# Optimization experiments

Measured on AMD Instinct MI355X. Metric: run time of the kernel, lower is better.

The kernel has to match this reference:

```python
import jax, jax.numpy as jnp
import numpy as np

N, E, B = 4096, 32768, 1024
NF, EF = 32, 16
ENC, HID, HEADS = 64, 128, 4  # hidden_dim = 2*encoder_dim
MAX_SIZE = 10


def setup_inputs() -> dict:
    key = jax.random.key(0)
    ks = jax.random.split(key, 11)
    return {
        "node_features": jax.random.normal(ks[0], (N, NF), jnp.float32),
        "edge_features": jax.random.normal(ks[1], (E, EF), jnp.float32),
        "edge_index": jax.random.randint(ks[2], (2, E), 0, N, jnp.int32),
        "current_state": jax.random.randint(ks[3], (B,), 0, N, jnp.int32),
        "n_states": jax.random.randint(ks[4], (N,), 1, MAX_SIZE + 1, jnp.int32),
        "W_h": jax.random.normal(ks[5], (NF, HID), jnp.float32) / np.sqrt(NF),
        "W_e": jax.random.normal(ks[6], (EF, HID), jnp.float32) / np.sqrt(EF),
        "W_a": jax.random.normal(ks[7], (5 * HID, HEADS * HID), jnp.float32) / np.sqrt(5 * HID),
        "W_m": jax.random.normal(ks[8], (3 * HID, HEADS * HID), jnp.float32) / np.sqrt(3 * HID),
        "a_kern": jax.random.normal(ks[9], (HID, 1), jnp.float32) / np.sqrt(HID),
        "W_g": jax.random.normal(ks[10], (HID, ENC), jnp.float32) / np.sqrt(HID),
    }


def reference(node_features, edge_features, edge_index, current_state, n_states,
              W_h, W_e, W_a, W_m, a_kern, W_g):
    n_nodes = node_features.shape[0]
    h0 = node_features @ W_h                        # [N, HID]
    e = edge_features @ W_e                         # [E, HID]
    attn_mask = jnp.any(edge_features != 0, axis=-1)  # [E]
    src, tgt = edge_index[0], edge_index[1]
    neg_inf = -jnp.inf
    h = h0
    for i in range(MAX_SIZE):
        node_in = jnp.concatenate([h, h0], axis=-1)  # [N, 2*HID]
        sf = node_in[src]                            # [E, 2*HID]
        tf = node_in[tgt]                            # [E, 2*HID]
        h_a = (jnp.concatenate([sf, e, tf], axis=-1) @ W_a).reshape(-1, HEADS, HID)
        h_m = (jnp.concatenate([e, tf], axis=-1) @ W_m).reshape(-1, HEADS, HID)
        logits = jax.nn.leaky_relu(h_a, 0.2) @ a_kern            # [E, HEADS, 1]
        logits = jnp.where(attn_mask[:, None, None], logits, neg_inf)
        max_per_node = jax.ops.segment_max(logits.reshape(logits.shape[0], -1), src,
                                           num_segments=n_nodes)  # [N, HEADS]
        dead = jnp.isneginf(max_per_node[:, 0])[src]              # [E]
        safe = jnp.where(dead[:, None, None], 0.0, logits)
        # segment softmax over edges grouped by src
        m = jax.ops.segment_max(safe.reshape(-1, HEADS), src, num_segments=n_nodes)
        ex = jnp.exp(safe - m[src][:, :, None])                   # [E, HEADS, 1]
        denom = jax.ops.segment_sum(ex, src, num_segments=n_nodes)
        attn = ex / denom[src]
        msgs = attn * h_m                                         # [E, HEADS, HID]
        agg = jax.ops.segment_sum(msgs, src, num_segments=n_nodes)  # [N, HEADS, HID]
        _h = jnp.tanh(agg.sum(axis=1))                            # [N, HID]
        h = jnp.where((i < n_states)[:, None], _h, h)
    return h[current_state] @ W_g                                 # [B, ENC]
```

## Files before the change

kernel.cpp:

```cpp
#include <hip/hip_runtime.h>
#include <hip/hip_bf16.h>

#define N_NODES 4096
#define N_EDGES 32768
#define BATCH   1024
#define NFEAT   32
#define EFEAT   16
#define ENCD    64
#define HIDD    128
#define HEADS   4
#define HID4    512
#define MAXS    10
#define TVAR    1536

typedef unsigned short ushort_t;
typedef __bf16 bf16x8 __attribute__((ext_vector_type(8)));
typedef float f32x4 __attribute__((ext_vector_type(4)));

static __device__ __forceinline__ float bfbits2f(unsigned int hi16) {
    return __uint_as_float(hi16);
}
static __device__ __forceinline__ void unpack8(uint4 v, float* f) {
    f[0] = bfbits2f(v.x << 16); f[1] = bfbits2f(v.x & 0xffff0000u);
    f[2] = bfbits2f(v.y << 16); f[3] = bfbits2f(v.y & 0xffff0000u);
    f[4] = bfbits2f(v.z << 16); f[5] = bfbits2f(v.z & 0xffff0000u);
    f[6] = bfbits2f(v.w << 16); f[7] = bfbits2f(v.w & 0xffff0000u);
}
static __device__ __forceinline__ void load8bf(const ushort_t* p, float* f) {
    unpack8(*reinterpret_cast<const uint4*>(p), f);
}
static __device__ __forceinline__ unsigned short f2bf(float x) {
    __hip_bfloat16 h = __float2bfloat16(x);
    return *reinterpret_cast<unsigned short*>(&h);
}
static __device__ __forceinline__ unsigned addpack(unsigned s, unsigned a) {
    float s0 = bfbits2f(s << 16), s1 = bfbits2f(s & 0xffff0000u);
    float a0 = bfbits2f(a << 16), a1 = bfbits2f(a & 0xffff0000u);
    unsigned r0 = f2bf(s0 + a0), r1 = f2bf(s1 + a1);
    return r0 | (r1 << 16);
}
static __device__ __forceinline__ uint4 pack8(const float* f) {
    uint4 u;
    u.x = (unsigned)f2bf(f[0]) | ((unsigned)f2bf(f[1]) << 16);
    u.y = (unsigned)f2bf(f[2]) | ((unsigned)f2bf(f[3]) << 16);
    u.z = (unsigned)f2bf(f[4]) | ((unsigned)f2bf(f[5]) << 16);
    u.w = (unsigned)f2bf(f[6]) | ((unsigned)f2bf(f[7]) << 16);
    return u;
}


__global__ __launch_bounds__(256) void k_comp_eam(const float* __restrict__ We,
                                                  const float* __restrict__ Wa,
                                                  const float* __restrict__ Wm,
                                                  ushort_t* __restrict__ out) {
    __shared__ float w_lds[128][17];
    const int t = threadIdx.x;
    const int p = blockIdx.x;
    const int cl = t & 15, kbase = t >> 4;
    const int c = p * 16 + cl;
#pragma unroll
    for (int i = 0; i < 8; ++i) {
        int kk = kbase + i * 16;
        w_lds[kk][cl] = (c < 512) ? Wa[(256 + kk) * HID4 + c] : Wm[kk * HID4 + (c - 512)];
    }
    __syncthreads();
    const int k = t >> 4;
    float s = 0.f;
    for (int kk = 0; kk < 128; ++kk)
        s = fmaf(We[k * 128 + kk], w_lds[kk][cl], s);
    int l = ((k >> 3) << 4) + cl, j = k & 7;
    out[((size_t)(p * 64 + l)) * 8 + j] = f2bf(s);
    if (t < 32) {
        uint4 z = {0, 0, 0, 0};
        *(uint4*)(out + ((size_t)(p * 64 + 32 + t)) * 8) = z;
    }
}

__global__ __launch_bounds__(256) void k_comp_fix(const float* __restrict__ Wh,
                                                  const float* __restrict__ Wa,
                                                  const float* __restrict__ Wm,
                                                  ushort_t* __restrict__ out) {
    __shared__ float w_lds[128][17];
    const int t = threadIdx.x;
    const int p = blockIdx.x;
    const int cl = t & 15, kbase = t >> 4;
    const int c = p * 16 + cl;
#pragma unroll
    for (int i = 0; i < 8; ++i) {
        int kk = kbase + i * 16;
        w_lds[kk][cl] = (c < 512) ? Wa[(128 + kk) * HID4 + c]
                      : (c < 1024) ? Wa[(512 + kk) * HID4 + (c - 512)]
                                   : Wm[(256 + kk) * HID4 + (c - 1024)];
    }
    __syncthreads();
    const int k1 = t >> 4, k2 = k1 + 16;
    float s1 = 0.f, s2 = 0.f;
    for (int kk = 0; kk < 128; ++kk) {
        float wv = w_lds[kk][cl];
        s1 = fmaf(Wh[k1 * 128 + kk], wv, s1);
        s2 = fmaf(Wh[k2 * 128 + kk], wv, s2);
    }
    int l1 = ((k1 >> 3) << 4) + cl, j1 = k1 & 7;
    int l2 = ((k2 >> 3) << 4) + cl, j2 = k2 & 7;
    out[((size_t)(p * 64 + l1)) * 8 + j1] = f2bf(s1);
    out[((size_t)(p * 64 + l2)) * 8 + j2] = f2bf(s2);
}

__global__ void k_pack_var(const float* __restrict__ Wa, const float* __restrict__ Wm,
                           ushort_t* __restrict__ out) {
    int idx = blockIdx.x * blockDim.x + threadIdx.x;
    int p = idx >> 8, rem = idx & 255;
    int q = rem >> 6, l = rem & 63;
    int c = p * 16 + (l & 15);
    int k0 = q * 32 + ((l >> 4) << 3);
    float v[8];
#pragma unroll
    for (int j = 0; j < 8; ++j) {
        int k = k0 + j;
        v[j] = (c < 512) ? Wa[k * HID4 + c]
             : (c < 1024) ? Wa[(384 + k) * HID4 + (c - 512)]
                          : Wm[(128 + k) * HID4 + (c - 1024)];
    }
    *(uint4*)(out + (size_t)idx * 8) = pack8(v);
}

__global__ void k_prep_ef(const float* __restrict__ ef, ushort_t* __restrict__ out) {
    int idx = blockIdx.x * blockDim.x + threadIdx.x;
    int p = idx >> 6, l = idx & 63;
    int e = p * 16 + (l & 15);
    int k0 = (l >> 4) << 3;
    float v[8];
#pragma unroll
    for (int j = 0; j < 8; ++j) {
        int k = k0 + j;
        v[j] = (k < 16) ? ef[e * EFEAT + k] : 0.f;
    }
    *(uint4*)(out + (size_t)idx * 8) = pack8(v);
}

__global__ void k_prep_nf(const float* __restrict__ nf, ushort_t* __restrict__ out) {
    int idx = blockIdx.x * blockDim.x + threadIdx.x;
    int p = idx >> 6, l = idx & 63;
    int n = p * 16 + (l & 15);
    int k0 = (l >> 4) << 3;
    float v[8];
#pragma unroll
    for (int j = 0; j < 8; ++j) v[j] = nf[n * NFEAT + k0 + j];
    *(uint4*)(out + (size_t)idx * 8) = pack8(v);
}

__global__ void k_h0(const float* __restrict__ nf, const float* __restrict__ Wh,
                     float* __restrict__ hA, ushort_t* __restrict__ hAbf) {
    int idx = blockIdx.x * blockDim.x + threadIdx.x;
    int n = idx >> 7, c = idx & 127;
    float s = 0.f;
#pragma unroll
    for (int k = 0; k < NFEAT; ++k) s += nf[n * NFEAT + k] * Wh[k * HIDD + c];
    hA[idx] = s;
    int p = n >> 4, r = n & 15, q = c >> 5, kg = (c >> 3) & 3, j = c & 7;
    hAbf[(size_t)(((p * 4 + q) * 64) + kg * 16 + r) * 8 + j] = f2bf(s);
}

__global__ void k_mask(const float* __restrict__ ef, int* __restrict__ mask) {
    int e = blockIdx.x * blockDim.x + threadIdx.x;
    int m = 0;
#pragma unroll
    for (int k = 0; k < EFEAT; ++k) m |= (ef[e * EFEAT + k] != 0.f);
    mask[e] = m;
}

__global__ __launch_bounds__(256) void k_gemm32(const ushort_t* __restrict__ A_sw,
                                                const ushort_t* __restrict__ B_sw,
                                                ushort_t* __restrict__ C, int NC) {
    __shared__ ushort_t lds[4][64][64];
    const int tid = threadIdx.x;
    const int l = tid & 63;
    const int w = tid >> 6;
    const int mpb = blockIdx.y * 16 + w * 4;
    const int cpb = blockIdx.x * 4;

    bf16x8 a[4], b[4];
#pragma unroll
    for (int mi = 0; mi < 4; ++mi)
        a[mi] = *(const bf16x8*)(A_sw + (size_t)((mpb + mi) * 64 + l) * 8);
#pragma unroll
    for (int ct = 0; ct < 4; ++ct)
        b[ct] = *(const bf16x8*)(B_sw + (size_t)((cpb + ct) * 64 + l) * 8);

    const int rb = (l >> 4) << 2, lc = l & 15;
#pragma unroll
    for (int mi = 0; mi < 4; ++mi)
#pragma unroll
        for (int ct = 0; ct < 4; ++ct) {
            f32x4 c = {0.f, 0.f, 0.f, 0.f};
            c = __builtin_amdgcn_mfma_f32_16x16x32_bf16(a[mi], b[ct], c, 0, 0, 0);
#pragma unroll
            for (int r = 0; r < 4; ++r)
                lds[w][mi * 16 + rb + r][ct * 16 + lc] = f2bf(c[r]);
        }
    __syncthreads();
#pragma unroll
    for (int i = 0; i < 8; ++i) {
        int ch = (i << 6) + l;
        int row = ch >> 3, co = (ch & 7) << 3;
        int grow = blockIdx.y * 256 + w * 64 + row;
        size_t gidx = (size_t)grow * NC + blockIdx.x * 64 + co;
        *(uint4*)(C + gidx) = *(const uint4*)(&lds[w][row][co]);
    }
}

__global__ __launch_bounds__(256) void k_gemm128(const ushort_t* __restrict__ A_sw,
                                                 const ushort_t* __restrict__ B_sw,
                                                 const ushort_t* __restrict__ Cadd,
                                                 ushort_t* __restrict__ C, int NC) {
    __shared__ ushort_t lds[4][32][64];
    const int tid = threadIdx.x;
    const int l = tid & 63;
    const int w = tid >> 6;
    const int mpb = blockIdx.y * 8 + w * 2;
    const int cpb = blockIdx.x * 4;

    bf16x8 a[2][4], b[4][4];
#pragma unroll
    for (int mi = 0; mi < 2; ++mi)
#pragma unroll
        for (int q = 0; q < 4; ++q)
            a[mi][q] = *(const bf16x8*)(A_sw + (size_t)(((mpb + mi) * 4 + q) * 64 + l) * 8);
#pragma unroll
    for (int ct = 0; ct < 4; ++ct)
#pragma unroll
        for (int q = 0; q < 4; ++q)
            b[ct][q] = *(const bf16x8*)(B_sw + (size_t)(((cpb + ct) * 4 + q) * 64 + l) * 8);

    const int rb = (l >> 4) << 2, lc = l & 15;
#pragma unroll
    for (int mi = 0; mi < 2; ++mi)
#pragma unroll
        for (int ct = 0; ct < 4; ++ct) {
            f32x4 c = {0.f, 0.f, 0.f, 0.f};
#pragma unroll
            for (int q = 0; q < 4; ++q)
                c = __builtin_amdgcn_mfma_f32_16x16x32_bf16(a[mi][q], b[ct][q], c, 0, 0, 0);
#pragma unroll
            for (int r = 0; r < 4; ++r)
                lds[w][mi * 16 + rb + r][ct * 16 + lc] = f2bf(c[r]);
        }
    __syncthreads();
#pragma unroll
    for (int i = 0; i < 4; ++i) {
        int ch = (i << 6) + l;
        int row = ch >> 3, co = (ch & 7) << 3;
        int grow = blockIdx.y * 128 + w * 32 + row;
        size_t gidx = (size_t)grow * NC + blockIdx.x * 64 + co;
        uint4 sv = *(const uint4*)(&lds[w][row][co]);
        uint4 av = *(const uint4*)(Cadd + gidx);
        sv.x = addpack(sv.x, av.x);
        sv.y = addpack(sv.y, av.y);
        sv.z = addpack(sv.z, av.z);
        sv.w = addpack(sv.w, av.w);
        *(uint4*)(C + gidx) = sv;
    }
}

__global__ void k_zero(int* p) { p[blockIdx.x * blockDim.x + threadIdx.x] = 0; }
__global__ void k_count(const int* __restrict__ src, int* __restrict__ deg) {
    int e = blockIdx.x * blockDim.x + threadIdx.x;
    atomicAdd(&deg[src[e]], 1);
}
__global__ __launch_bounds__(1024) void k_scan(const int* __restrict__ deg,
                                               int* __restrict__ offs, int* __restrict__ cursor) {
    __shared__ int sm[1024];
    int t = threadIdx.x;
    int d0 = deg[t * 4], d1 = deg[t * 4 + 1], d2 = deg[t * 4 + 2], d3 = deg[t * 4 + 3];
    int s = d0 + d1 + d2 + d3;
    sm[t] = s; __syncthreads();
    for (int o = 1; o < 1024; o <<= 1) {
        int v = (t >= o) ? sm[t - o] : 0;
        __syncthreads();
        sm[t] += v;
        __syncthreads();
    }
    int run = sm[t] - s;
    offs[t * 4] = run;     cursor[t * 4] = run;     run += d0;
    offs[t * 4 + 1] = run; cursor[t * 4 + 1] = run; run += d1;
    offs[t * 4 + 2] = run; cursor[t * 4 + 2] = run; run += d2;
    offs[t * 4 + 3] = run; cursor[t * 4 + 3] = run;
    if (t == 1023) offs[4096] = run + d3;
}
__global__ void k_fill(const int* __restrict__ src, int* __restrict__ cursor, int* __restrict__ eids) {
    int e = blockIdx.x * blockDim.x + threadIdx.x;
    int pos = atomicAdd(&cursor[src[e]], 1);
    eids[pos] = e;
}

__global__ __launch_bounds__(256) void k_edge(const ushort_t* __restrict__ T,
                                              const ushort_t* __restrict__ eam,
                                              const int* __restrict__ tgt,
                                              const int* __restrict__ offs,
                                              const int* __restrict__ eids,
                                              const int* __restrict__ mask,
                                              const float* __restrict__ a_kern,
                                              const int* __restrict__ n_states,
                                              const float* __restrict__ h_old,
                                              float* __restrict__ h_new,
                                              ushort_t* __restrict__ h_new_bf, int iter) {
    const int n = (blockIdx.x << 2) + (threadIdx.x >> 6);
    const int lane = threadIdx.x & 63;
    const int c0 = lane << 3;
    const int e0 = offs[n], e1 = offs[n + 1];

    float ak[8];
    {
        const float4* p = reinterpret_cast<const float4*>(a_kern + ((lane & 15) << 3));
        float4 a0 = p[0], a1 = p[1];
        ak[0] = a0.x; ak[1] = a0.y; ak[2] = a0.z; ak[3] = a0.w;
        ak[4] = a1.x; ak[5] = a1.y; ak[6] = a1.z; ak[7] = a1.w;
    }
    float asrc[8];
    load8bf(T + (size_t)n * TVAR + c0, asrc);

    float m = -INFINITY, s = 0.f;
    float acc[8] = {0, 0, 0, 0, 0, 0, 0, 0};

    int mk_n = 0;
    uint4 va_n, vt_n, vm_n, vtm_n;
    if (e0 < e1) {
        int e = eids[e0]; int t = tgt[e]; mk_n = mask[e];
        va_n  = *(const uint4*)(eam + (size_t)e * 1024 + c0);
        vt_n  = *(const uint4*)(T + (size_t)t * TVAR + 512 + c0);
        vm_n  = *(const uint4*)(eam + (size_t)e * 1024 + 512 + c0);
        vtm_n = *(const uint4*)(T + (size_t)t * TVAR + 1024 + c0);
    }
    for (int q = e0; q < e1; ++q) {
        uint4 va = va_n, vt = vt_n, vm = vm_n, vtm = vtm_n;
        int mk = mk_n;
        int q2 = q + 1;
        if (q2 < e1) {
            int e = eids[q2]; int t = tgt[e]; mk_n = mask[e];
            va_n  = *(const uint4*)(eam + (size_t)e * 1024 + c0);
            vt_n  = *(const uint4*)(T + (size_t)t * TVAR + 512 + c0);
            vm_n  = *(const uint4*)(eam + (size_t)e * 1024 + 512 + c0);
            vtm_n = *(const uint4*)(T + (size_t)t * TVAR + 1024 + c0);
        }
        float ea[8], tt[8], em[8], tm[8];
        unpack8(va, ea); unpack8(vt, tt); unpack8(vm, em); unpack8(vtm, tm);
        float p = 0.f;
#pragma unroll
        for (int j = 0; j < 8; ++j) {
            float v = asrc[j] + ea[j] + tt[j];
            v = (v > 0.f) ? v : 0.2f * v;
            p = fmaf(v, ak[j], p);
        }
        p += __shfl_xor(p, 1);
        p += __shfl_xor(p, 2);
        p += __shfl_xor(p, 4);
        p += __shfl_xor(p, 8);
        p = mk ? p : -INFINITY;
        float mn = fmaxf(m, p);
        bool live = (mn != -INFINITY);
        float wgt = live ? __expf(p - mn) : 0.f;
        float sc  = live ? __expf(m - mn) : 0.f;
        s = s * sc + wgt;
#pragma unroll
        for (int j = 0; j < 8; ++j) acc[j] = acc[j] * sc + wgt * (em[j] + tm[j]);
        m = mn;
    }
    if (e1 > e0 && m == -INFINITY) {
        s = (float)(e1 - e0);
        for (int q = e0; q < e1; ++q) {
            int e = eids[q]; int t = tgt[e];
            float em[8], tm[8];
            load8bf(eam + (size_t)e * 1024 + 512 + c0, em);
            load8bf(T + (size_t)t * TVAR + 1024 + c0, tm);
#pragma unroll
            for (int j = 0; j < 8; ++j) acc[j] += em[j] + tm[j];
        }
    }
    float inv = (e1 > e0) ? (1.f / s) : 0.f;
    float r[8];
#pragma unroll
    for (int j = 0; j < 8; ++j) {
        float v = acc[j] * inv;
        v += __shfl_xor(v, 16);
        v += __shfl_xor(v, 32);
        r[j] = v;
    }
    bool upd = iter < n_states[n];
    if (lane < 16) {
        float out[8];
#pragma unroll
        for (int j = 0; j < 8; ++j)
            out[j] = upd ? tanhf(r[j]) : h_old[(size_t)n * HIDD + c0 + j];
        float4* ph = reinterpret_cast<float4*>(h_new + (size_t)n * HIDD + c0);
        float4 o0, o1;
        o0.x = out[0]; o0.y = out[1]; o0.z = out[2]; o0.w = out[3];
        o1.x = out[4]; o1.y = out[5]; o1.z = out[6]; o1.w = out[7];
        ph[0] = o0; ph[1] = o1;
        int p = n >> 4, rr = n & 15, q = lane >> 2, kg = lane & 3;
        *(uint4*)(h_new_bf + (size_t)(((p * 4 + q) * 64) + kg * 16 + rr) * 8) = pack8(out);
    }
}

__global__ void k_out(const float* __restrict__ h, const int* __restrict__ cs,
                      const float* __restrict__ Wg, float* __restrict__ out) {
    int idx = blockIdx.x * blockDim.x + threadIdx.x;
    int b = idx >> 6, c = idx & 63;
    int n = cs[b];
    float s = 0.f;
#pragma unroll
    for (int k = 0; k < HIDD; ++k) s += h[(size_t)n * HIDD + k] * Wg[k * ENCD + c];
    out[idx] = s;
}

extern "C" void kernel_launch(void* const* d_in, const int* in_sizes, int n_in,
                              void* d_out, int out_size, void* d_ws, size_t ws_size,
                              hipStream_t stream) {
    const float* nf  = (const float*)d_in[0];
    const float* ef  = (const float*)d_in[1];
    const int* eidx  = (const int*)d_in[2];
    const int* cs    = (const int*)d_in[3];
    const int* nst   = (const int*)d_in[4];
    const float* Wh  = (const float*)d_in[5];
    const float* We  = (const float*)d_in[6];
    const float* Wa  = (const float*)d_in[7];
    const float* Wm  = (const float*)d_in[8];
    const float* akn = (const float*)d_in[9];
    const float* Wg  = (const float*)d_in[10];
    const int* src = eidx;
    const int* tgt = eidx + N_EDGES;

    char* w = (char*)d_ws;
    size_t off = 0;
    auto alloc = [&](size_t bytes) -> void* {
        void* p = w + off;
        off = (off + bytes + 255) & ~(size_t)255;
        return p;
    };
    float* hA        = (float*)alloc((size_t)N_NODES * HIDD * 4);
    float* hB        = (float*)alloc((size_t)N_NODES * HIDD * 4);
    ushort_t* hAbf   = (ushort_t*)alloc((size_t)N_NODES * HIDD * 2);
    ushort_t* hBbf   = (ushort_t*)alloc((size_t)N_NODES * HIDD * 2);
    int* mask        = (int*)alloc((size_t)N_EDGES * 4);
    ushort_t* eam    = (ushort_t*)alloc((size_t)N_EDGES * 1024 * 2);
    ushort_t* Tfix   = (ushort_t*)alloc((size_t)N_NODES * TVAR * 2);
    ushort_t* Tcur   = (ushort_t*)alloc((size_t)N_NODES * TVAR * 2);
    ushort_t* Wcomb  = (ushort_t*)alloc((size_t)64 * 64 * 8 * 2);
    ushort_t* WfixC  = (ushort_t*)alloc((size_t)96 * 64 * 8 * 2);
    ushort_t* WvarSw = (ushort_t*)alloc((size_t)96 * 4 * 64 * 8 * 2);
    ushort_t* efp    = (ushort_t*)alloc((size_t)2048 * 64 * 8 * 2);
    ushort_t* nfp    = (ushort_t*)alloc((size_t)256 * 64 * 8 * 2);
    int* deg         = (int*)alloc((size_t)N_NODES * 4);
    int* offs        = (int*)alloc((size_t)(N_NODES + 1) * 4);
    int* cursor      = (int*)alloc((size_t)N_NODES * 4);
    int* eids        = (int*)alloc((size_t)N_EDGES * 4);
    (void)ws_size; (void)in_sizes; (void)n_in; (void)out_size;

    k_comp_eam<<<64, 256, 0, stream>>>(We, Wa, Wm, Wcomb);
    k_comp_fix<<<96, 256, 0, stream>>>(Wh, Wa, Wm, WfixC);
    k_pack_var<<<96, 256, 0, stream>>>(Wa, Wm, WvarSw);
    k_prep_ef<<<512, 256, 0, stream>>>(ef, efp);
    k_prep_nf<<<64, 256, 0, stream>>>(nf, nfp);
    k_h0<<<(N_NODES * HIDD) / 256, 256, 0, stream>>>(nf, Wh, hA, hAbf);
    k_mask<<<N_EDGES / 256, 256, 0, stream>>>(ef, mask);

    k_gemm32<<<dim3(1024 / 64, N_EDGES / 256), 256, 0, stream>>>(efp, Wcomb, eam, 1024);
    k_gemm32<<<dim3(TVAR / 64, N_NODES / 256), 256, 0, stream>>>(nfp, WfixC, Tfix, TVAR);

    k_zero<<<N_NODES / 256, 256, 0, stream>>>(deg);
    k_count<<<N_EDGES / 256, 256, 0, stream>>>(src, deg);
    k_scan<<<1, 1024, 0, stream>>>(deg, offs, cursor);
    k_fill<<<N_EDGES / 256, 256, 0, stream>>>(src, cursor, eids);

    float* hcur = hA; float* hnext = hB;
    ushort_t* hcbf = hAbf; ushort_t* hnbf = hBbf;
    for (int i = 0; i < MAXS; ++i) {
        k_gemm128<<<dim3(TVAR / 64, N_NODES / 128), 256, 0, stream>>>(hcbf, WvarSw, Tfix, Tcur, TVAR);
        k_edge<<<N_NODES / 4, 256, 0, stream>>>(Tcur, eam, tgt, offs, eids, mask, akn, nst,
                                                hcur, hnext, hnbf, i);
        float* tmp = hcur; hcur = hnext; hnext = tmp;
        ushort_t* tb = hcbf; hcbf = hnbf; hnbf = tb;
    }
    k_out<<<(BATCH * ENCD) / 256, 256, 0, stream>>>(hcur, cs, Wg, (float*)d_out);
}
```

Before: 497.6 us.

## Sort nodes by n_states bucket and skip inactive nodes each iteration

Nodes are permuted so that the ones with more remaining iterations come first, and edges are renumbered in the permuted CSR order. Each iteration's node GEMM and edge kernel then exit early for row blocks and nodes whose n_states no longer allow an update, and the h buffers are updated in place instead of double-buffered. Edge data (eam, tgt, mask) is stored in CSR order, which makes the edge-feature reads contiguous and removes the eids indirection. This adds several small preprocessing kernels with atomics. It relies on frozen nodes never being rewritten, so that in-place updates stay correct.

```diff
diff --git a/kernel.cpp b/kernel.cpp
--- a/kernel.cpp
+++ b/kernel.cpp
@@ -49,6 +49,28 @@
 }
 
 
+__global__ void k_zero(int* p) { p[blockIdx.x * blockDim.x + threadIdx.x] = 0; }
+__global__ void k_bcount(const int* __restrict__ nst, int* __restrict__ bcnt) {
+    int n = blockIdx.x * blockDim.x + threadIdx.x;
+    atomicAdd(&bcnt[10 - nst[n]], 1);
+}
+__global__ void k_bprefix(const int* __restrict__ bcnt, int* __restrict__ bcur,
+                          int* __restrict__ cntAct) {
+    if (threadIdx.x == 0) {
+        int boffs[11]; int run = 0;
+        for (int b = 0; b < 10; ++b) { boffs[b] = run; run += bcnt[b]; }
+        boffs[10] = run;
+        for (int b = 0; b < 10; ++b) bcur[b] = boffs[b];
+        for (int i = 0; i < 10; ++i) cntAct[i] = boffs[10 - i];
+    }
+}
+__global__ void k_bscatter(const int* __restrict__ nst, int* __restrict__ bcur,
+                           int* __restrict__ perm, int* __restrict__ inv) {
+    int n = blockIdx.x * blockDim.x + threadIdx.x;
+    int pos = atomicAdd(&bcur[10 - nst[n]], 1);
+    perm[pos] = n; inv[n] = pos;
+}
+
 __global__ __launch_bounds__(256) void k_comp_eam(const float* __restrict__ We,
                                                   const float* __restrict__ Wa,
                                                   const float* __restrict__ Wm,
@@ -124,10 +146,11 @@
     *(uint4*)(out + (size_t)idx * 8) = pack8(v);
 }
 
-__global__ void k_prep_ef(const float* __restrict__ ef, ushort_t* __restrict__ out) {
+__global__ void k_prep_ef(const float* __restrict__ ef, const int* __restrict__ eids,
+                          ushort_t* __restrict__ out) {
     int idx = blockIdx.x * blockDim.x + threadIdx.x;
     int p = idx >> 6, l = idx & 63;
-    int e = p * 16 + (l & 15);
+    int e = eids[p * 16 + (l & 15)];
     int k0 = (l >> 4) << 3;
     float v[8];
 #pragma unroll
@@ -138,10 +161,11 @@
     *(uint4*)(out + (size_t)idx * 8) = pack8(v);
 }
 
-__global__ void k_prep_nf(const float* __restrict__ nf, ushort_t* __restrict__ out) {
+__global__ void k_prep_nf(const float* __restrict__ nf, const int* __restrict__ perm,
+                          ushort_t* __restrict__ out) {
     int idx = blockIdx.x * blockDim.x + threadIdx.x;
     int p = idx >> 6, l = idx & 63;
-    int n = p * 16 + (l & 15);
+    int n = perm[p * 16 + (l & 15)];
     int k0 = (l >> 4) << 3;
     float v[8];
 #pragma unroll
@@ -150,15 +174,17 @@
 }
 
 __global__ void k_h0(const float* __restrict__ nf, const float* __restrict__ Wh,
-                     float* __restrict__ hA, ushort_t* __restrict__ hAbf) {
+                     const int* __restrict__ inv,
+                     float* __restrict__ h, ushort_t* __restrict__ hbf) {
     int idx = blockIdx.x * blockDim.x + threadIdx.x;
     int n = idx >> 7, c = idx & 127;
     float s = 0.f;
 #pragma unroll
     for (int k = 0; k < NFEAT; ++k) s += nf[n * NFEAT + k] * Wh[k * HIDD + c];
-    hA[idx] = s;
-    int p = n >> 4, r = n & 15, q = c >> 5, kg = (c >> 3) & 3, j = c & 7;
-    hAbf[(size_t)(((p * 4 + q) * 64) + kg * 16 + r) * 8 + j] = f2bf(s);
+    int row = inv[n];
+    h[(size_t)row * HIDD + c] = s;
+    int p = row >> 4, r = row & 15, q = c >> 5, kg = (c >> 3) & 3, j = c & 7;
+    hbf[(size_t)(((p * 4 + q) * 64) + kg * 16 + r) * 8 + j] = f2bf(s);
 }
 
 __global__ void k_mask(const float* __restrict__ ef, int* __restrict__ mask) {
@@ -167,6 +193,46 @@
 #pragma unroll
     for (int k = 0; k < EFEAT; ++k) m |= (ef[e * EFEAT + k] != 0.f);
     mask[e] = m;
+}
+
+__global__ void k_count(const int* __restrict__ src, const int* __restrict__ inv,
+                        int* __restrict__ deg) {
+    int e = blockIdx.x * blockDim.x + threadIdx.x;
+    atomicAdd(&deg[inv[src[e]]], 1);
+}
+__global__ __launch_bounds__(1024) void k_scan(const int* __restrict__ deg,
+                                               int* __restrict__ offs, int* __restrict__ cursor) {
+    __shared__ int sm[1024];
+    int t = threadIdx.x;
+    int d0 = deg[t * 4], d1 = deg[t * 4 + 1], d2 = deg[t * 4 + 2], d3 = deg[t * 4 + 3];
+    int s = d0 + d1 + d2 + d3;
+    sm[t] = s; __syncthreads();
+    for (int o = 1; o < 1024; o <<= 1) {
+        int v = (t >= o) ? sm[t - o] : 0;
+        __syncthreads();
+        sm[t] += v;
+        __syncthreads();
+    }
+    int run = sm[t] - s;
+    offs[t * 4] = run;     cursor[t * 4] = run;     run += d0;
+    offs[t * 4 + 1] = run; cursor[t * 4 + 1] = run; run += d1;
+    offs[t * 4 + 2] = run; cursor[t * 4 + 2] = run; run += d2;
+    offs[t * 4 + 3] = run; cursor[t * 4 + 3] = run;
+    if (t == 1023) offs[4096] = run + d3;
+}
+__global__ void k_fill(const int* __restrict__ src, const int* __restrict__ inv,
+                       int* __restrict__ cursor, int* __restrict__ eids) {
+    int e = blockIdx.x * blockDim.x + threadIdx.x;
+    int pos = atomicAdd(&cursor[inv[src[e]]], 1);
+    eids[pos] = e;
+}
+__global__ void k_tgtp(const int* __restrict__ eids, const int* __restrict__ tgt,
+                       const int* __restrict__ inv, const int* __restrict__ mask,
+                       int* __restrict__ tgtp, int* __restrict__ maskp) {
+    int q = blockIdx.x * blockDim.x + threadIdx.x;
+    int e = eids[q];
+    tgtp[q] = inv[tgt[e]];
+    maskp[q] = mask[e];
 }
 
 __global__ __launch_bounds__(256) void k_gemm32(const ushort_t* __restrict__ A_sw,
@@ -212,7 +278,11 @@
 __global__ __launch_bounds__(256) void k_gemm128(const ushort_t* __restrict__ A_sw,
                                                  const ushort_t* __restrict__ B_sw,
                                                  const ushort_t* __restrict__ Cadd,
-                                                 ushort_t* __restrict__ C, int NC) {
+                                                 ushort_t* __restrict__ C, int NC,
+                                                 const int* __restrict__ cntAct, int iter) {
+    const int thr = (iter == 0) ? N_NODES : cntAct[iter - 1];
+    if ((int)(blockIdx.y * 128) >= thr) return;
+
     __shared__ ushort_t lds[4][32][64];
     const int tid = threadIdx.x;
     const int l = tid & 63;
@@ -262,49 +332,18 @@
     }
 }
 
-__global__ void k_zero(int* p) { p[blockIdx.x * blockDim.x + threadIdx.x] = 0; }
-__global__ void k_count(const int* __restrict__ src, int* __restrict__ deg) {
-    int e = blockIdx.x * blockDim.x + threadIdx.x;
-    atomicAdd(&deg[src[e]], 1);
-}
-__global__ __launch_bounds__(1024) void k_scan(const int* __restrict__ deg,
-                                               int* __restrict__ offs, int* __restrict__ cursor) {
-    __shared__ int sm[1024];
-    int t = threadIdx.x;
-    int d0 = deg[t * 4], d1 = deg[t * 4 + 1], d2 = deg[t * 4 + 2], d3 = deg[t * 4 + 3];
-    int s = d0 + d1 + d2 + d3;
-    sm[t] = s; __syncthreads();
-    for (int o = 1; o < 1024; o <<= 1) {
-        int v = (t >= o) ? sm[t - o] : 0;
-        __syncthreads();
-        sm[t] += v;
-        __syncthreads();
-    }
-    int run = sm[t] - s;
-    offs[t * 4] = run;     cursor[t * 4] = run;     run += d0;
-    offs[t * 4 + 1] = run; cursor[t * 4 + 1] = run; run += d1;
-    offs[t * 4 + 2] = run; cursor[t * 4 + 2] = run; run += d2;
-    offs[t * 4 + 3] = run; cursor[t * 4 + 3] = run;
-    if (t == 1023) offs[4096] = run + d3;
-}
-__global__ void k_fill(const int* __restrict__ src, int* __restrict__ cursor, int* __restrict__ eids) {
-    int e = blockIdx.x * blockDim.x + threadIdx.x;
-    int pos = atomicAdd(&cursor[src[e]], 1);
-    eids[pos] = e;
-}
-
 __global__ __launch_bounds__(256) void k_edge(const ushort_t* __restrict__ T,
                                               const ushort_t* __restrict__ eam,
-                                              const int* __restrict__ tgt,
+                                              const int* __restrict__ tgtp,
                                               const int* __restrict__ offs,
-                                              const int* __restrict__ eids,
-                                              const int* __restrict__ mask,
+                                              const int* __restrict__ maskp,
                                               const float* __restrict__ a_kern,
-                                              const int* __restrict__ n_states,
-                                              const float* __restrict__ h_old,
-                                              float* __restrict__ h_new,
-                                              ushort_t* __restrict__ h_new_bf, int iter) {
+                                              const int* __restrict__ cntAct,
+                                              float* __restrict__ h,
+                                              ushort_t* __restrict__ hbf, int iter) {
     const int n = (blockIdx.x << 2) + (threadIdx.x >> 6);
+    if (n >= cntAct[iter]) return;
+
     const int lane = threadIdx.x & 63;
     const int c0 = lane << 3;
     const int e0 = offs[n], e1 = offs[n + 1];
@@ -325,10 +364,10 @@
     int mk_n = 0;
     uint4 va_n, vt_n, vm_n, vtm_n;
     if (e0 < e1) {
-        int e = eids[e0]; int t = tgt[e]; mk_n = mask[e];
-        va_n  = *(const uint4*)(eam + (size_t)e * 1024 + c0);
+        int t = tgtp[e0]; mk_n = maskp[e0];
+        va_n  = *(const uint4*)(eam + (size_t)e0 * 1024 + c0);
         vt_n  = *(const uint4*)(T + (size_t)t * TVAR + 512 + c0);
-        vm_n  = *(const uint4*)(eam + (size_t)e * 1024 + 512 + c0);
+        vm_n  = *(const uint4*)(eam + (size_t)e0 * 1024 + 512 + c0);
         vtm_n = *(const uint4*)(T + (size_t)t * TVAR + 1024 + c0);
     }
     for (int q = e0; q < e1; ++q) {
@@ -336,10 +375,10 @@
         int mk = mk_n;
         int q2 = q + 1;
         if (q2 < e1) {
-            int e = eids[q2]; int t = tgt[e]; mk_n = mask[e];
-            va_n  = *(const uint4*)(eam + (size_t)e * 1024 + c0);
+            int t = tgtp[q2]; mk_n = maskp[q2];
+            va_n  = *(const uint4*)(eam + (size_t)q2 * 1024 + c0);
             vt_n  = *(const uint4*)(T + (size_t)t * TVAR + 512 + c0);
-            vm_n  = *(const uint4*)(eam + (size_t)e * 1024 + 512 + c0);
+            vm_n  = *(const uint4*)(eam + (size_t)q2 * 1024 + 512 + c0);
             vtm_n = *(const uint4*)(T + (size_t)t * TVAR + 1024 + c0);
         }
         float ea[8], tt[8], em[8], tm[8];
@@ -368,44 +407,43 @@
     if (e1 > e0 && m == -INFINITY) {
         s = (float)(e1 - e0);
         for (int q = e0; q < e1; ++q) {
-            int e = eids[q]; int t = tgt[e];
+            int t = tgtp[q];
             float em[8], tm[8];
-            load8bf(eam + (size_t)e * 1024 + 512 + c0, em);
+            load8bf(eam + (size_t)q * 1024 + 512 + c0, em);
             load8bf(T + (size_t)t * TVAR + 1024 + c0, tm);
 #pragma unroll
             for (int j = 0; j < 8; ++j) acc[j] += em[j] + tm[j];
         }
     }
-    float inv = (e1 > e0) ? (1.f / s) : 0.f;
+    float inv_s = (e1 > e0) ? (1.f / s) : 0.f;
     float r[8];
 #pragma unroll
     for (int j = 0; j < 8; ++j) {
-        float v = acc[j] * inv;
+        float v = acc[j] * inv_s;
         v += __shfl_xor(v, 16);
         v += __shfl_xor(v, 32);
         r[j] = v;
     }
-    bool upd = iter < n_states[n];
     if (lane < 16) {
         float out[8];
 #pragma unroll
-        for (int j = 0; j < 8; ++j)
-            out[j] = upd ? tanhf(r[j]) : h_old[(size_t)n * HIDD + c0 + j];
-        float4* ph = reinterpret_cast<float4*>(h_new + (size_t)n * HIDD + c0);
+        for (int j = 0; j < 8; ++j) out[j] = tanhf(r[j]);
+        float4* ph = reinterpret_cast<float4*>(h + (size_t)n * HIDD + c0);
         float4 o0, o1;
         o0.x = out[0]; o0.y = out[1]; o0.z = out[2]; o0.w = out[3];
         o1.x = out[4]; o1.y = out[5]; o1.z = out[6]; o1.w = out[7];
         ph[0] = o0; ph[1] = o1;
         int p = n >> 4, rr = n & 15, q = lane >> 2, kg = lane & 3;
-        *(uint4*)(h_new_bf + (size_t)(((p * 4 + q) * 64) + kg * 16 + rr) * 8) = pack8(out);
+        *(uint4*)(hbf + (size_t)(((p * 4 + q) * 64) + kg * 16 + rr) * 8) = pack8(out);
     }
 }
 
 __global__ void k_out(const float* __restrict__ h, const int* __restrict__ cs,
-                      const float* __restrict__ Wg, float* __restrict__ out) {
+                      const int* __restrict__ inv, const float* __restrict__ Wg,
+                      float* __restrict__ out) {
     int idx = blockIdx.x * blockDim.x + threadIdx.x;
     int b = idx >> 6, c = idx & 63;
-    int n = cs[b];
+    int n = inv[cs[b]];
     float s = 0.f;
 #pragma unroll
     for (int k = 0; k < HIDD; ++k) s += h[(size_t)n * HIDD + k] * Wg[k * ENCD + c];
@@ -436,10 +474,8 @@
         off = (off + bytes + 255) & ~(size_t)255;
         return p;
     };
-    float* hA        = (float*)alloc((size_t)N_NODES * HIDD * 4);
-    float* hB        = (float*)alloc((size_t)N_NODES * HIDD * 4);
-    ushort_t* hAbf   = (ushort_t*)alloc((size_t)N_NODES * HIDD * 2);
-    ushort_t* hBbf   = (ushort_t*)alloc((size_t)N_NODES * HIDD * 2);
+    float* h         = (float*)alloc((size_t)N_NODES * HIDD * 4);
+    ushort_t* hbf    = (ushort_t*)alloc((size_t)N_NODES * HIDD * 2);
     int* mask        = (int*)alloc((size_t)N_EDGES * 4);
     ushort_t* eam    = (ushort_t*)alloc((size_t)N_EDGES * 1024 * 2);
     ushort_t* Tfix   = (ushort_t*)alloc((size_t)N_NODES * TVAR * 2);
@@ -449,36 +485,45 @@
     ushort_t* WvarSw = (ushort_t*)alloc((size_t)96 * 4 * 64 * 8 * 2);
     ushort_t* efp    = (ushort_t*)alloc((size_t)2048 * 64 * 8 * 2);
     ushort_t* nfp    = (ushort_t*)alloc((size_t)256 * 64 * 8 * 2);
-    int* deg         = (int*)alloc((size_t)N_NODES * 4);
+    int* iws         = (int*)alloc((size_t)4352 * 4);
+    int* deg    = iws;
+    int* bcnt   = iws + 4096;
+    int* bcur   = iws + 4112;
+    int* cntAct = iws + 4128;
     int* offs        = (int*)alloc((size_t)(N_NODES + 1) * 4);
     int* cursor      = (int*)alloc((size_t)N_NODES * 4);
+    int* perm        = (int*)alloc((size_t)N_NODES * 4);
+    int* inv         = (int*)alloc((size_t)N_NODES * 4);
     int* eids        = (int*)alloc((size_t)N_EDGES * 4);
+    int* tgtp        = (int*)alloc((size_t)N_EDGES * 4);
+    int* maskp       = (int*)alloc((size_t)N_EDGES * 4);
     (void)ws_size; (void)in_sizes; (void)n_in; (void)out_size;
+
+    k_zero<<<17, 256, 0, stream>>>(iws);
+    k_bcount<<<N_NODES / 256, 256, 0, stream>>>(nst, bcnt);
+    k_bprefix<<<1, 64, 0, stream>>>(bcnt, bcur, cntAct);
+    k_bscatter<<<N_NODES / 256, 256, 0, stream>>>(nst, bcur, perm, inv);
+    k_mask<<<N_EDGES / 256, 256, 0, stream>>>(ef, mask);
+    k_count<<<N_EDGES / 256, 256, 0, stream>>>(src, inv, deg);
+    k_scan<<<1, 1024, 0, stream>>>(deg, offs, cursor);
+    k_fill<<<N_EDGES / 256, 256, 0, stream>>>(src, inv, cursor, eids);
+    k_tgtp<<<N_EDGES / 256, 256, 0, stream>>>(eids, tgt, inv, mask, tgtp, maskp);
 
     k_comp_eam<<<64, 256, 0, stream>>>(We, Wa, Wm, Wcomb);
     k_comp_fix<<<96, 256, 0, stream>>>(Wh, Wa, Wm, WfixC);
     k_pack_var<<<96, 256, 0, stream>>>(Wa, Wm, WvarSw);
-    k_prep_ef<<<512, 256, 0, stream>>>(ef, efp);
-    k_prep_nf<<<64, 256, 0, stream>>>(nf, nfp);
-    k_h0<<<(N_NODES * HIDD) / 256, 256, 0, stream>>>(nf, Wh, hA, hAbf);
-    k_mask<<<N_EDGES / 256, 256, 0, stream>>>(ef, mask);
+    k_prep_ef<<<512, 256, 0, stream>>>(ef, eids, efp);
+    k_prep_nf<<<64, 256, 0, stream>>>(nf, perm, nfp);
+    k_h0<<<(N_NODES * HIDD) / 256, 256, 0, stream>>>(nf, Wh, inv, h, hbf);
 
     k_gemm32<<<dim3(1024 / 64, N_EDGES / 256), 256, 0, stream>>>(efp, Wcomb, eam, 1024);
     k_gemm32<<<dim3(TVAR / 64, N_NODES / 256), 256, 0, stream>>>(nfp, WfixC, Tfix, TVAR);
 
-    k_zero<<<N_NODES / 256, 256, 0, stream>>>(deg);
-    k_count<<<N_EDGES / 256, 256, 0, stream>>>(src, deg);
-    k_scan<<<1, 1024, 0, stream>>>(deg, offs, cursor);
-    k_fill<<<N_EDGES / 256, 256, 0, stream>>>(src, cursor, eids);
-
-    float* hcur = hA; float* hnext = hB;
-    ushort_t* hcbf = hAbf; ushort_t* hnbf = hBbf;
     for (int i = 0; i < MAXS; ++i) {
-        k_gemm128<<<dim3(TVAR / 64, N_NODES / 128), 256, 0, stream>>>(hcbf, WvarSw, Tfix, Tcur, TVAR);
-        k_edge<<<N_NODES / 4, 256, 0, stream>>>(Tcur, eam, tgt, offs, eids, mask, akn, nst,
-                                                hcur, hnext, hnbf, i);
-        float* tmp = hcur; hcur = hnext; hnext = tmp;
-        ushort_t* tb = hcbf; hcbf = hnbf; hnbf = tb;
-    }
-    k_out<<<(BATCH * ENCD) / 256, 256, 0, stream>>>(hcur, cs, Wg, (float*)d_out);
-}
+        k_gemm128<<<dim3(TVAR / 64, N_NODES / 128), 256, 0, stream>>>(hbf, WvarSw, Tfix, Tcur,
+                                                                      TVAR, cntAct, i);
+        k_edge<<<N_NODES / 4, 256, 0, stream>>>(Tcur, eam, tgtp, offs, maskp, akn, cntAct,
+                                                h, hbf, i);
+    }
+    k_out<<<(BATCH * ENCD) / 256, 256, 0, stream>>>(h, cs, inv, Wg, (float*)d_out);
+}
```

Measured after the change: 444.6 us. 10.6% less time.
